# Optimization experiments

Hardware: AMD Instinct MI355X
Metric: run time of the kernel (lower is better)

Reference implementation:

```python
import jax, jax.numpy as jnp
import numpy as np

B, T1, T2 = 16, 1024, 1024
K1D, K2D, V1D, V2D, A = 512, 512, 256, 256, 128


def setup_inputs() -> dict:
    key = jax.random.key(0)
    ks = jax.random.split(key, 10)
    inp = {
        "k1": jax.random.normal(ks[0], (B, T1, K1D), dtype=jnp.float32),
        "k2": jax.random.normal(ks[1], (B, T2, K2D), dtype=jnp.float32),
        "v1": jax.random.normal(ks[2], (B, T1, V1D), dtype=jnp.float32),
        "v2": jax.random.normal(ks[3], (B, T2, V2D), dtype=jnp.float32),
        # Linear params (torch nn.Linear: y = x @ W.T + b)
        "W1": jax.random.normal(ks[4], (A, K1D), dtype=jnp.float32) / np.sqrt(K1D),
        "b1": jnp.zeros((A,), dtype=jnp.float32),
        "W2": jax.random.normal(ks[5], (A, K2D), dtype=jnp.float32) / np.sqrt(K2D),
        "b2": jnp.zeros((A,), dtype=jnp.float32),
        # valid lengths in [T/2, T-1] so no softmax row is entirely -inf
        "k1_lengths": jax.random.randint(ks[6], (B,), T1 // 2, T1, dtype=jnp.int32),
        "k2_lengths": jax.random.randint(ks[7], (B,), T2 // 2, T2, dtype=jnp.int32),
    }
    return inp


def reference(k1, k2, v1, v2, W1, b1, W2, b2, k1_lengths, k2_lengths):
    # projections
    q1 = jnp.einsum("bti,ai->bta", k1, W1) + b1  # [B,T1,A]
    q2 = jnp.einsum("bti,ai->bta", k2, W2) + b2  # [B,T2,A]
    # co-attention score [B,T1,T2]
    score = jnp.einsum("bia,bja->bij", q1, q2)
    # faithful mask: torch code adds 1 for rows>=l1 and 1 for cols>=l2,
    # then masks where sum == 1  -> XOR of the two pad conditions.
    row_pad = jnp.arange(T1)[None, :, None] >= k1_lengths[:, None, None]  # [B,T1,1]
    col_pad = jnp.arange(T2)[None, None, :] >= k2_lengths[:, None, None]  # [B,1,T2]
    mask = jnp.logical_xor(row_pad, col_pad)
    score = jnp.where(mask, -jnp.inf, score)
    # dual softmaxes
    w1 = jax.nn.softmax(jnp.swapaxes(score, 1, 2), axis=-1)  # [B,T2,T1]
    w2 = jax.nn.softmax(score, axis=-1)                      # [B,T1,T2]
    o1 = jnp.einsum("bji,bid->bjd", w1, v1)  # [B,T2,V1D]
    o2 = jnp.einsum("bij,bjd->bid", w2, v2)  # [B,T1,V2D]
    # note: the torch module additionally slices w1/w2/score per sample to
    # (l2,l1)/(l1,l2) ragged views; with fixed shapes we return the full
    # tensors (the valid region matches; slicing is a zero-copy view in torch).
    return (o1, o2, w1, w2, score)
```

## Files before the change

kernel.cpp:

```cpp
#include <hip/hip_runtime.h>
#include <math.h>

namespace {
constexpr int TT   = 1024;
constexpr int AD   = 128;
constexpr int KDIM = 512;
constexpr int VDIM = 256;
constexpr int NB   = 16;
constexpr size_t T2T = (size_t)TT * TT;
constexpr size_t BT  = (size_t)NB * TT;
}

#define MASK_VAL (-1.0e30f)

typedef __bf16 bf16x8 __attribute__((ext_vector_type(8)));
typedef float  f32x4  __attribute__((ext_vector_type(4)));

__device__ __forceinline__ unsigned short bf16_rne(float x) {
    unsigned int u = __builtin_bit_cast(unsigned int, x);
    u += 0x7fffu + ((u >> 16) & 1u);
    return (unsigned short)(u >> 16);
}
__device__ __forceinline__ float bf16f(unsigned short h) {
    return __builtin_bit_cast(float, ((unsigned int)h) << 16);
}
__device__ __forceinline__ void split2(float x, unsigned short& h, unsigned short& l) {
    h = bf16_rne(x);
    l = bf16_rne(x - bf16f(h));
}

__global__ __launch_bounds__(256) void prep_vt_kernel(
    const float* __restrict__ v1, const float* __restrict__ v2,
    unsigned short* __restrict__ vth, unsigned short* __restrict__ vtl)
{
    const int b     = blockIdx.x;
    const int k0    = blockIdx.y * 32;
    const int which = blockIdx.z;
    const float* vb = (which ? v1 : v2) + (size_t)b * TT * VDIM;
    const int tid = threadIdx.x;

    __shared__ float ls[32][257];
#pragma unroll
    for (int rep = 0; rep < 8; ++rep) {
        int idx = tid + rep * 256;
        int k  = idx >> 6;
        int n4 = (idx & 63) * 4;
        float4 x = *(const float4*)(vb + (size_t)(k0 + k) * VDIM + n4);
        ls[k][n4 + 0] = x.x;
        ls[k][n4 + 1] = x.y;
        ls[k][n4 + 2] = x.z;
        ls[k][n4 + 3] = x.w;
    }
    __syncthreads();

    const size_t pbase = ((size_t)(which * NB + b)) * VDIM * TT;
#pragma unroll
    for (int rep = 0; rep < 4; ++rep) {
        int idx = tid + rep * 256;
        int n  = idx >> 2;
        int sg = (idx & 3) * 8;
        unsigned short h[8], l[8];
#pragma unroll
        for (int j = 0; j < 8; ++j) {
            float x = ls[sg + j][n];
            split2(x, h[j], l[j]);
        }
        uint4 H, L;
        H.x = (unsigned)h[0] | ((unsigned)h[1] << 16);
        H.y = (unsigned)h[2] | ((unsigned)h[3] << 16);
        H.z = (unsigned)h[4] | ((unsigned)h[5] << 16);
        H.w = (unsigned)h[6] | ((unsigned)h[7] << 16);
        L.x = (unsigned)l[0] | ((unsigned)l[1] << 16);
        L.y = (unsigned)l[2] | ((unsigned)l[3] << 16);
        L.z = (unsigned)l[4] | ((unsigned)l[5] << 16);
        L.w = (unsigned)l[6] | ((unsigned)l[7] << 16);
        size_t off = pbase + (size_t)n * TT + k0 + sg;
        *(uint4*)(vth + off) = H;
        *(uint4*)(vtl + off) = L;
    }
}

__global__ __launch_bounds__(256) void qproj_mfma_kernel(
    const float* __restrict__ k1, const float* __restrict__ W1, const float* __restrict__ bias1,
    const float* __restrict__ k2, const float* __restrict__ W2, const float* __restrict__ bias2,
    unsigned short* __restrict__ q1h, unsigned short* __restrict__ q1l,
    unsigned short* __restrict__ q2h, unsigned short* __restrict__ q2l)
{
    const int proj = blockIdx.y;
    const float* __restrict__ K    = proj ? k2 : k1;
    const float* __restrict__ W    = proj ? W2 : W1;
    const float* __restrict__ bias = proj ? bias2 : bias1;
    unsigned short* __restrict__ qh = proj ? q2h : q1h;
    unsigned short* __restrict__ ql = proj ? q2l : q1l;

    const int m0 = blockIdx.x * 128;

    __shared__ alignas(16) unsigned short akh[128 * 40];
    __shared__ alignas(16) unsigned short akl[128 * 40];
    __shared__ alignas(16) unsigned short bwh[128 * 40];
    __shared__ alignas(16) unsigned short bwl[128 * 40];

    const int tid  = threadIdx.x;
    const int lane = tid & 63;
    const int wv   = tid >> 6;
    const int wm = wv >> 1, wn = wv & 1;
    const int la = lane & 15, kg = lane >> 4;

    f32x4 acc[4][4];
#pragma unroll
    for (int m = 0; m < 4; ++m)
#pragma unroll
        for (int n = 0; n < 4; ++n) acc[m][n] = (f32x4){0.f, 0.f, 0.f, 0.f};

    for (int k0 = 0; k0 < KDIM; k0 += 32) {
#pragma unroll
        for (int rep = 0; rep < 4; ++rep) {
            int idx = tid + rep * 256;
            int row = idx >> 3, c4 = (idx & 7) * 4;
            float4 x = *(const float4*)(K + (size_t)(m0 + row) * KDIM + k0 + c4);
            ushort4 H, L;
            split2(x.x, H.x, L.x);
            split2(x.y, H.y, L.y);
            split2(x.z, H.z, L.z);
            split2(x.w, H.w, L.w);
            *(ushort4*)&akh[row * 40 + c4] = H;
            *(ushort4*)&akl[row * 40 + c4] = L;
        }
#pragma unroll
        for (int rep = 0; rep < 4; ++rep) {
            int idx = tid + rep * 256;
            int row = idx >> 3, c4 = (idx & 7) * 4;
            float4 x = *(const float4*)(W + (size_t)row * KDIM + k0 + c4);
            ushort4 H, L;
            split2(x.x, H.x, L.x);
            split2(x.y, H.y, L.y);
            split2(x.z, H.z, L.z);
            split2(x.w, H.w, L.w);
            *(ushort4*)&bwh[row * 40 + c4] = H;
            *(ushort4*)&bwl[row * 40 + c4] = L;
        }
        __syncthreads();

        bf16x8 ah[4], al[4], bh[4], bl[4];
#pragma unroll
        for (int m = 0; m < 4; ++m) {
            int r = wm * 64 + m * 16 + la;
            ah[m] = *(const bf16x8*)&akh[r * 40 + kg * 8];
            al[m] = *(const bf16x8*)&akl[r * 40 + kg * 8];
        }
#pragma unroll
        for (int n = 0; n < 4; ++n) {
            int c = wn * 64 + n * 16 + la;
            bh[n] = *(const bf16x8*)&bwh[c * 40 + kg * 8];
            bl[n] = *(const bf16x8*)&bwl[c * 40 + kg * 8];
        }
#pragma unroll
        for (int m = 0; m < 4; ++m)
#pragma unroll
            for (int n = 0; n < 4; ++n) {
                acc[m][n] = __builtin_amdgcn_mfma_f32_16x16x32_bf16(ah[m], bh[n], acc[m][n], 0, 0, 0);
                acc[m][n] = __builtin_amdgcn_mfma_f32_16x16x32_bf16(ah[m], bl[n], acc[m][n], 0, 0, 0);
                acc[m][n] = __builtin_amdgcn_mfma_f32_16x16x32_bf16(al[m], bh[n], acc[m][n], 0, 0, 0);
            }
        __syncthreads();
    }

#pragma unroll
    for (int n = 0; n < 4; ++n) {
        int col = wn * 64 + n * 16 + la;
        float bv = bias[col];
#pragma unroll
        for (int m = 0; m < 4; ++m)
#pragma unroll
            for (int r = 0; r < 4; ++r) {
                int row = m0 + wm * 64 + m * 16 + kg * 4 + r;
                unsigned short h, l;
                split2(acc[m][n][r] + bv, h, l);
                qh[(size_t)row * AD + col] = h;
                ql[(size_t)row * AD + col] = l;
            }
    }
}

__global__ __launch_bounds__(256) void score_mfma_stats_kernel(
    const unsigned short* __restrict__ q1h, const unsigned short* __restrict__ q1l,
    const unsigned short* __restrict__ q2h, const unsigned short* __restrict__ q2l,
    const int* __restrict__ len1, const int* __restrict__ len2,
    float* __restrict__ score,
    float* __restrict__ prm, float* __restrict__ prs,
    float* __restrict__ pcm, float* __restrict__ pcs)
{
    const int b  = blockIdx.x;
    const int mt = blockIdx.y >> 3, nt = blockIdx.y & 7;
    const int m0 = mt * 128, n0 = nt * 128;
    const size_t qoff = (size_t)b * TT * AD;

    __shared__ alignas(16) unsigned short ath[128 * 40];
    __shared__ alignas(16) unsigned short atl[128 * 40];
    __shared__ alignas(16) unsigned short bth[128 * 40];
    __shared__ alignas(16) unsigned short btl[128 * 40];
    __shared__ float red_m[2][128];
    __shared__ float red_s[2][128];

    const int tid  = threadIdx.x;
    const int lane = tid & 63;
    const int wv   = tid >> 6;
    const int wm = wv >> 1, wn = wv & 1;
    const int la = lane & 15, kg = lane >> 4;

    f32x4 acc[4][4];
#pragma unroll
    for (int m = 0; m < 4; ++m)
#pragma unroll
        for (int n = 0; n < 4; ++n) acc[m][n] = (f32x4){0.f, 0.f, 0.f, 0.f};

    for (int k0 = 0; k0 < AD; k0 += 32) {
#pragma unroll
        for (int rep = 0; rep < 2; ++rep) {
            int idx = tid + rep * 256;
            int row = idx >> 2, sg = (idx & 3) * 8;
            *(uint4*)&ath[row * 40 + sg] = *(const uint4*)(q1h + qoff + (size_t)(m0 + row) * AD + k0 + sg);
            *(uint4*)&atl[row * 40 + sg] = *(const uint4*)(q1l + qoff + (size_t)(m0 + row) * AD + k0 + sg);
            *(uint4*)&bth[row * 40 + sg] = *(const uint4*)(q2h + qoff + (size_t)(n0 + row) * AD + k0 + sg);
            *(uint4*)&btl[row * 40 + sg] = *(const uint4*)(q2l + qoff + (size_t)(n0 + row) * AD + k0 + sg);
        }
        __syncthreads();

        bf16x8 ah[4], al[4], bh[4], bl[4];
#pragma unroll
        for (int m = 0; m < 4; ++m) {
            int r = wm * 64 + m * 16 + la;
            ah[m] = *(const bf16x8*)&ath[r * 40 + kg * 8];
            al[m] = *(const bf16x8*)&atl[r * 40 + kg * 8];
        }
#pragma unroll
        for (int n = 0; n < 4; ++n) {
            int c = wn * 64 + n * 16 + la;
            bh[n] = *(const bf16x8*)&bth[c * 40 + kg * 8];
            bl[n] = *(const bf16x8*)&btl[c * 40 + kg * 8];
        }
#pragma unroll
        for (int m = 0; m < 4; ++m)
#pragma unroll
            for (int n = 0; n < 4; ++n) {
                acc[m][n] = __builtin_amdgcn_mfma_f32_16x16x32_bf16(ah[m], bh[n], acc[m][n], 0, 0, 0);
                acc[m][n] = __builtin_amdgcn_mfma_f32_16x16x32_bf16(ah[m], bl[n], acc[m][n], 0, 0, 0);
                acc[m][n] = __builtin_amdgcn_mfma_f32_16x16x32_bf16(al[m], bh[n], acc[m][n], 0, 0, 0);
            }
        __syncthreads();
    }

    const int l1v = len1[b];
    const int l2v = len2[b];

#pragma unroll
    for (int m = 0; m < 4; ++m)
#pragma unroll
        for (int r = 0; r < 4; ++r) {
            int row = m0 + wm * 64 + m * 16 + kg * 4 + r;
            bool rp = row >= l1v;
#pragma unroll
            for (int n = 0; n < 4; ++n) {
                int col = n0 + wn * 64 + n * 16 + la;
                bool cp = col >= l2v;
                if (rp != cp) acc[m][n][r] = MASK_VAL;
            }
        }
    float* sb = score + (size_t)b * T2T;
#pragma unroll
    for (int m = 0; m < 4; ++m)
#pragma unroll
        for (int r = 0; r < 4; ++r) {
            int row = m0 + wm * 64 + m * 16 + kg * 4 + r;
#pragma unroll
            for (int n = 0; n < 4; ++n) {
                int col = n0 + wn * 64 + n * 16 + la;
                sb[(size_t)row * TT + col] = acc[m][n][r];
            }
        }

#pragma unroll
    for (int m = 0; m < 4; ++m)
#pragma unroll
        for (int r = 0; r < 4; ++r) {
            float mr = fmaxf(fmaxf(acc[m][0][r], acc[m][1][r]),
                             fmaxf(acc[m][2][r], acc[m][3][r]));
#pragma unroll
            for (int off = 1; off <= 8; off <<= 1) mr = fmaxf(mr, __shfl_xor(mr, off));
            float sr = __expf(acc[m][0][r] - mr) + __expf(acc[m][1][r] - mr) +
                       __expf(acc[m][2][r] - mr) + __expf(acc[m][3][r] - mr);
#pragma unroll
            for (int off = 1; off <= 8; off <<= 1) sr += __shfl_xor(sr, off);
            if (la == 0) {
                int rloc = wm * 64 + m * 16 + kg * 4 + r;
                red_m[wn][rloc] = mr;
                red_s[wn][rloc] = sr;
            }
        }
    __syncthreads();
    if (tid < 128) {
        float ma = red_m[0][tid], mb2 = red_m[1][tid];
        float mm = fmaxf(ma, mb2);
        float ss = red_s[0][tid] * __expf(ma - mm) + red_s[1][tid] * __expf(mb2 - mm);
        prm[(size_t)nt * BT + (size_t)b * TT + m0 + tid] = mm;
        prs[(size_t)nt * BT + (size_t)b * TT + m0 + tid] = ss;
    }
    __syncthreads();

#pragma unroll
    for (int n = 0; n < 4; ++n) {
        float mc = MASK_VAL;
#pragma unroll
        for (int m = 0; m < 4; ++m)
#pragma unroll
            for (int r = 0; r < 4; ++r) mc = fmaxf(mc, acc[m][n][r]);
#pragma unroll
        for (int off = 16; off <= 32; off <<= 1) mc = fmaxf(mc, __shfl_xor(mc, off));
        float sc = 0.f;
#pragma unroll
        for (int m = 0; m < 4; ++m)
#pragma unroll
            for (int r = 0; r < 4; ++r) sc += __expf(acc[m][n][r] - mc);
#pragma unroll
        for (int off = 16; off <= 32; off <<= 1) sc += __shfl_xor(sc, off);
        if (kg == 0) {
            int cloc = wn * 64 + n * 16 + la;
            red_m[wm][cloc] = mc;
            red_s[wm][cloc] = sc;
        }
    }
    __syncthreads();
    if (tid < 128) {
        float ma = red_m[0][tid], mb2 = red_m[1][tid];
        float mm = fmaxf(ma, mb2);
        float ss = red_s[0][tid] * __expf(ma - mm) + red_s[1][tid] * __expf(mb2 - mm);
        pcm[(size_t)mt * BT + (size_t)b * TT + n0 + tid] = mm;
        pcs[(size_t)mt * BT + (size_t)b * TT + n0 + tid] = ss;
    }
}

__global__ __launch_bounds__(256) void statcomb_kernel(
    const float* __restrict__ prm, const float* __restrict__ prs,
    const float* __restrict__ pcm, const float* __restrict__ pcs,
    float* __restrict__ rmax, float* __restrict__ rinv,
    float* __restrict__ cmax, float* __restrict__ cinv)
{
    const int id = blockIdx.x * 256 + threadIdx.x;
    const float* pm = blockIdx.y ? pcm : prm;
    const float* ps = blockIdx.y ? pcs : prs;
    float* om = blockIdx.y ? cmax : rmax;
    float* oi = blockIdx.y ? cinv : rinv;
    float nm = MASK_VAL;
#pragma unroll
    for (int c = 0; c < 8; ++c) nm = fmaxf(nm, pm[(size_t)c * BT + id]);
    float s = 0.f;
#pragma unroll
    for (int c = 0; c < 8; ++c)
        s += ps[(size_t)c * BT + id] * __expf(pm[(size_t)c * BT + id] - nm);
    om[id] = nm;
    oi[id] = 1.f / s;
}

__global__ __launch_bounds__(512) void ogemm_fused_kernel(
    const float* __restrict__ score,
    const float* __restrict__ rmax, const float* __restrict__ rinv,
    const float* __restrict__ cmax, const float* __restrict__ cinv,
    const unsigned short* __restrict__ vth, const unsigned short* __restrict__ vtl,
    float* __restrict__ w2, float* __restrict__ w1,
    float* __restrict__ o2, float* __restrict__ o1)
{
    const int b     = blockIdx.x;
    const int m0    = blockIdx.y * 128;
    const int which = blockIdx.z;
    const size_t vbase = ((size_t)(which * NB + b)) * VDIM * TT;

    const float* __restrict__ sb = score + (size_t)b * T2T;
    float* __restrict__ wout = (which ? w1 : w2) + (size_t)b * T2T;
    float* __restrict__ ob   = (which ? o1 : o2) + (size_t)b * TT * VDIM;

    __shared__ alignas(16) unsigned short awh[128 * 40];
    __shared__ alignas(16) unsigned short awl[128 * 40];
    __shared__ alignas(16) unsigned short bvh[256 * 40];
    __shared__ alignas(16) unsigned short bvl[256 * 40];
    __shared__ float st[128][33];
    __shared__ float sm_s[128], si_s[128];

    const int tid  = threadIdx.x;
    const int lane = tid & 63;
    const int wv   = tid >> 6;
    const int wm   = wv >> 2;
    const int wn   = wv & 3;
    const int la = lane & 15, kg = lane >> 4;

    if (tid < 128) {
        sm_s[tid] = (which ? cmax : rmax)[(size_t)b * TT + m0 + tid];
        si_s[tid] = (which ? cinv : rinv)[(size_t)b * TT + m0 + tid];
    }
    __syncthreads();

    f32x4 acc[4][4];
#pragma unroll
    for (int m = 0; m < 4; ++m)
#pragma unroll
        for (int n = 0; n < 4; ++n) acc[m][n] = (f32x4){0.f, 0.f, 0.f, 0.f};

    for (int k0 = 0; k0 < TT; k0 += 32) {
        if (which == 0) {
#pragma unroll
            for (int rep = 0; rep < 2; ++rep) {
                int idx = tid + rep * 512;
                int row = idx >> 3, c4 = (idx & 7) * 4;
                float4 x = *(const float4*)(sb + (size_t)(m0 + row) * TT + k0 + c4);
                float mm = sm_s[row], ii = si_s[row];
                f32x4 wv4;
                wv4[0] = __expf(x.x - mm) * ii;
                wv4[1] = __expf(x.y - mm) * ii;
                wv4[2] = __expf(x.z - mm) * ii;
                wv4[3] = __expf(x.w - mm) * ii;
                __builtin_nontemporal_store(wv4, (f32x4*)(wout + (size_t)(m0 + row) * TT + k0 + c4));
                ushort4 H, L;
                split2(wv4[0], H.x, L.x);
                split2(wv4[1], H.y, L.y);
                split2(wv4[2], H.z, L.z);
                split2(wv4[3], H.w, L.w);
                *(ushort4*)&awh[row * 40 + c4] = H;
                *(ushort4*)&awl[row * 40 + c4] = L;
            }
        } else {
#pragma unroll
            for (int rep = 0; rep < 2; ++rep) {
                int idx = tid + rep * 512;
                int ip = idx >> 5, c4 = (idx & 31) * 4;
                float4 x = *(const float4*)(sb + (size_t)(k0 + ip) * TT + m0 + c4);
                st[c4 + 0][ip] = __expf(x.x - sm_s[c4 + 0]) * si_s[c4 + 0];
                st[c4 + 1][ip] = __expf(x.y - sm_s[c4 + 1]) * si_s[c4 + 1];
                st[c4 + 2][ip] = __expf(x.z - sm_s[c4 + 2]) * si_s[c4 + 2];
                st[c4 + 3][ip] = __expf(x.w - sm_s[c4 + 3]) * si_s[c4 + 3];
            }
            __syncthreads();
#pragma unroll
            for (int rep = 0; rep < 2; ++rep) {
                int idx = tid + rep * 512;
                int j = idx >> 3, i4 = (idx & 7) * 4;
                f32x4 wv4;
                wv4[0] = st[j][i4 + 0];
                wv4[1] = st[j][i4 + 1];
                wv4[2] = st[j][i4 + 2];
                wv4[3] = st[j][i4 + 3];
                __builtin_nontemporal_store(wv4, (f32x4*)(wout + (size_t)(m0 + j) * TT + k0 + i4));
                ushort4 H, L;
                split2(wv4[0], H.x, L.x);
                split2(wv4[1], H.y, L.y);
                split2(wv4[2], H.z, L.z);
                split2(wv4[3], H.w, L.w);
                *(ushort4*)&awh[j * 40 + i4] = H;
                *(ushort4*)&awl[j * 40 + i4] = L;
            }
        }
#pragma unroll
        for (int rep = 0; rep < 2; ++rep) {
            int idx = tid + rep * 512;
            int n  = idx >> 2;
            int sg = (idx & 3) * 8;
            size_t off = vbase + (size_t)n * TT + k0 + sg;
            *(uint4*)&bvh[n * 40 + sg] = *(const uint4*)(vth + off);
            *(uint4*)&bvl[n * 40 + sg] = *(const uint4*)(vtl + off);
        }
        __syncthreads();

        bf16x8 ah[4], al[4], bh[4], bl[4];
#pragma unroll
        for (int m = 0; m < 4; ++m) {
            int r = wm * 64 + m * 16 + la;
            ah[m] = *(const bf16x8*)&awh[r * 40 + kg * 8];
            al[m] = *(const bf16x8*)&awl[r * 40 + kg * 8];
        }
#pragma unroll
        for (int n = 0; n < 4; ++n) {
            int c = wn * 64 + n * 16 + la;
            bh[n] = *(const bf16x8*)&bvh[c * 40 + kg * 8];
            bl[n] = *(const bf16x8*)&bvl[c * 40 + kg * 8];
        }
#pragma unroll
        for (int m = 0; m < 4; ++m)
#pragma unroll
            for (int n = 0; n < 4; ++n) {
                acc[m][n] = __builtin_amdgcn_mfma_f32_16x16x32_bf16(ah[m], bh[n], acc[m][n], 0, 0, 0);
                acc[m][n] = __builtin_amdgcn_mfma_f32_16x16x32_bf16(ah[m], bl[n], acc[m][n], 0, 0, 0);
                acc[m][n] = __builtin_amdgcn_mfma_f32_16x16x32_bf16(al[m], bh[n], acc[m][n], 0, 0, 0);
            }
        __syncthreads();
    }

#pragma unroll
    for (int m = 0; m < 4; ++m)
#pragma unroll
        for (int r = 0; r < 4; ++r) {
            int row = m0 + wm * 64 + m * 16 + kg * 4 + r;
#pragma unroll
            for (int n = 0; n < 4; ++n) {
                int col = wn * 64 + n * 16 + la;
                __builtin_nontemporal_store(acc[m][n][r], ob + (size_t)row * VDIM + col);
            }
        }
}

extern "C" void kernel_launch(void* const* d_in, const int* in_sizes, int n_in,
                              void* d_out, int out_size, void* d_ws, size_t ws_size,
                              hipStream_t stream) {
    const float* k1 = (const float*)d_in[0];
    const float* k2 = (const float*)d_in[1];
    const float* v1 = (const float*)d_in[2];
    const float* v2 = (const float*)d_in[3];
    const float* W1 = (const float*)d_in[4];
    const float* b1 = (const float*)d_in[5];
    const float* W2 = (const float*)d_in[6];
    const float* b2 = (const float*)d_in[7];
    const int* len1 = (const int*)d_in[8];
    const int* len2 = (const int*)d_in[9];

    float* out = (float*)d_out;
    float* o1    = out;
    float* o2    = out + (size_t)NB * TT * VDIM;
    float* w1    = out + (size_t)2 * NB * TT * VDIM;
    float* w2    = w1 + (size_t)NB * T2T;
    float* score = w2 + (size_t)NB * T2T;

    float* ws   = (float*)d_ws;
    float* rmax = ws;
    float* rinv = rmax + BT;
    float* cmax = rinv + BT;
    float* cinv = cmax + BT;
    float* prm  = cinv + BT;
    float* prs  = prm + 8 * BT;
    float* pcm  = prs + 8 * BT;
    float* pcs  = pcm + 8 * BT;
    unsigned short* q1h = (unsigned short*)(pcs + 8 * BT);
    unsigned short* q1l = q1h + BT * AD;
    unsigned short* q2h = q1l + BT * AD;
    unsigned short* q2l = q2h + BT * AD;
    unsigned short* vth = q2l + BT * AD;
    unsigned short* vtl = vth + (size_t)32 * VDIM * TT;

    prep_vt_kernel<<<dim3(NB, TT / 32, 2), 256, 0, stream>>>(v1, v2, vth, vtl);
    qproj_mfma_kernel<<<dim3(NB * TT / 128, 2), 256, 0, stream>>>(k1, W1, b1, k2, W2, b2,
                                                                  q1h, q1l, q2h, q2l);
    score_mfma_stats_kernel<<<dim3(NB, 64), 256, 0, stream>>>(q1h, q1l, q2h, q2l,
                                                              len1, len2, score,
                                                              prm, prs, pcm, pcs);
    statcomb_kernel<<<dim3(BT / 256, 2), 256, 0, stream>>>(prm, prs, pcm, pcs,
                                                           rmax, rinv, cmax, cinv);
    ogemm_fused_kernel<<<dim3(NB, TT / 128, 2), 512, 0, stream>>>(score, rmax, rinv, cmax, cinv,
                                                                  vth, vtl, w2, w1, o2, o1);
}
```

Baseline: 179.5 us.

## Load MFMA operands directly from global and software-prefetch score and V tiles

The score kernel now loads the q1/q2 hi/lo bf16 fragments straight from global memory into registers instead of staging them through LDS. This removes the per-step shared-memory round trips and barriers. In the output kernel the V^T hi/lo fragments are likewise read directly into registers, and both the score tile and the V fragments for the next k-step are issued one iteration ahead so their latency overlaps the current exp and MFMA work. This adds register pressure, and the global reads are duplicated across waves (each wave loads its own fragments, so there is less reuse than with shared staging).

```diff
diff --git a/kernel.cpp b/kernel.cpp
--- a/kernel.cpp
+++ b/kernel.cpp
@@ -27,6 +27,9 @@
 __device__ __forceinline__ void split2(float x, unsigned short& h, unsigned short& l) {
     h = bf16_rne(x);
     l = bf16_rne(x - bf16f(h));
+}
+__device__ __forceinline__ bf16x8 as_bf16x8(uint4 u) {
+    return __builtin_bit_cast(bf16x8, u);
 }
 
 __global__ __launch_bounds__(256) void prep_vt_kernel(
@@ -195,10 +198,6 @@
     const int m0 = mt * 128, n0 = nt * 128;
     const size_t qoff = (size_t)b * TT * AD;
 
-    __shared__ alignas(16) unsigned short ath[128 * 40];
-    __shared__ alignas(16) unsigned short atl[128 * 40];
-    __shared__ alignas(16) unsigned short bth[128 * 40];
-    __shared__ alignas(16) unsigned short btl[128 * 40];
     __shared__ float red_m[2][128];
     __shared__ float red_s[2][128];
 
@@ -214,30 +213,20 @@
 #pragma unroll
         for (int n = 0; n < 4; ++n) acc[m][n] = (f32x4){0.f, 0.f, 0.f, 0.f};
 
+#pragma unroll
     for (int k0 = 0; k0 < AD; k0 += 32) {
-#pragma unroll
-        for (int rep = 0; rep < 2; ++rep) {
-            int idx = tid + rep * 256;
-            int row = idx >> 2, sg = (idx & 3) * 8;
-            *(uint4*)&ath[row * 40 + sg] = *(const uint4*)(q1h + qoff + (size_t)(m0 + row) * AD + k0 + sg);
-            *(uint4*)&atl[row * 40 + sg] = *(const uint4*)(q1l + qoff + (size_t)(m0 + row) * AD + k0 + sg);
-            *(uint4*)&bth[row * 40 + sg] = *(const uint4*)(q2h + qoff + (size_t)(n0 + row) * AD + k0 + sg);
-            *(uint4*)&btl[row * 40 + sg] = *(const uint4*)(q2l + qoff + (size_t)(n0 + row) * AD + k0 + sg);
-        }
-        __syncthreads();
-
         bf16x8 ah[4], al[4], bh[4], bl[4];
 #pragma unroll
         for (int m = 0; m < 4; ++m) {
-            int r = wm * 64 + m * 16 + la;
-            ah[m] = *(const bf16x8*)&ath[r * 40 + kg * 8];
-            al[m] = *(const bf16x8*)&atl[r * 40 + kg * 8];
+            size_t off = qoff + (size_t)(m0 + wm * 64 + m * 16 + la) * AD + k0 + kg * 8;
+            ah[m] = as_bf16x8(*(const uint4*)(q1h + off));
+            al[m] = as_bf16x8(*(const uint4*)(q1l + off));
         }
 #pragma unroll
         for (int n = 0; n < 4; ++n) {
-            int c = wn * 64 + n * 16 + la;
-            bh[n] = *(const bf16x8*)&bth[c * 40 + kg * 8];
-            bl[n] = *(const bf16x8*)&btl[c * 40 + kg * 8];
+            size_t off = qoff + (size_t)(n0 + wn * 64 + n * 16 + la) * AD + k0 + kg * 8;
+            bh[n] = as_bf16x8(*(const uint4*)(q2h + off));
+            bl[n] = as_bf16x8(*(const uint4*)(q2l + off));
         }
 #pragma unroll
         for (int m = 0; m < 4; ++m)
@@ -247,7 +236,6 @@
                 acc[m][n] = __builtin_amdgcn_mfma_f32_16x16x32_bf16(ah[m], bl[n], acc[m][n], 0, 0, 0);
                 acc[m][n] = __builtin_amdgcn_mfma_f32_16x16x32_bf16(al[m], bh[n], acc[m][n], 0, 0, 0);
             }
-        __syncthreads();
     }
 
     const int l1v = len1[b];
@@ -380,8 +368,6 @@
 
     __shared__ alignas(16) unsigned short awh[128 * 40];
     __shared__ alignas(16) unsigned short awl[128 * 40];
-    __shared__ alignas(16) unsigned short bvh[256 * 40];
-    __shared__ alignas(16) unsigned short bvl[256 * 40];
     __shared__ float st[128][33];
     __shared__ float sm_s[128], si_s[128];
 
@@ -392,6 +378,11 @@
     const int wn   = wv & 3;
     const int la = lane & 15, kg = lane >> 4;
 
+    const int r_row0 = tid >> 3,          r_c4_0 = (tid & 7) * 4;
+    const int r_row1 = (tid + 512) >> 3,  r_c4_1 = ((tid + 512) & 7) * 4;
+    const int c_ip0 = tid >> 5,           c_c4_0 = (tid & 31) * 4;
+    const int c_ip1 = (tid + 512) >> 5,   c_c4_1 = ((tid + 512) & 31) * 4;
+
     if (tid < 128) {
         sm_s[tid] = (which ? cmax : rmax)[(size_t)b * TT + m0 + tid];
         si_s[tid] = (which ? cinv : rinv)[(size_t)b * TT + m0 + tid];
@@ -404,13 +395,37 @@
 #pragma unroll
         for (int n = 0; n < 4; ++n) acc[m][n] = (f32x4){0.f, 0.f, 0.f, 0.f};
 
+    float4 aA0, aA1;
+    uint4  bhr[4], blr[4];
+
+    auto issueA = [&](int k0) {
+        if (which == 0) {
+            aA0 = *(const float4*)(sb + (size_t)(m0 + r_row0) * TT + k0 + r_c4_0);
+            aA1 = *(const float4*)(sb + (size_t)(m0 + r_row1) * TT + k0 + r_c4_1);
+        } else {
+            aA0 = *(const float4*)(sb + (size_t)(k0 + c_ip0) * TT + m0 + c_c4_0);
+            aA1 = *(const float4*)(sb + (size_t)(k0 + c_ip1) * TT + m0 + c_c4_1);
+        }
+    };
+    auto issueB = [&](int k0) {
+#pragma unroll
+        for (int n = 0; n < 4; ++n) {
+            size_t off = vbase + (size_t)(wn * 64 + n * 16 + la) * TT + k0 + kg * 8;
+            bhr[n] = *(const uint4*)(vth + off);
+            blr[n] = *(const uint4*)(vtl + off);
+        }
+    };
+
+    issueA(0);
+    issueB(0);
+
     for (int k0 = 0; k0 < TT; k0 += 32) {
         if (which == 0) {
 #pragma unroll
             for (int rep = 0; rep < 2; ++rep) {
-                int idx = tid + rep * 512;
-                int row = idx >> 3, c4 = (idx & 7) * 4;
-                float4 x = *(const float4*)(sb + (size_t)(m0 + row) * TT + k0 + c4);
+                float4 x = rep ? aA1 : aA0;
+                int row = rep ? r_row1 : r_row0;
+                int c4  = rep ? r_c4_1 : r_c4_0;
                 float mm = sm_s[row], ii = si_s[row];
                 f32x4 wv4;
                 wv4[0] = __expf(x.x - mm) * ii;
@@ -426,17 +441,22 @@
                 *(ushort4*)&awh[row * 40 + c4] = H;
                 *(ushort4*)&awl[row * 40 + c4] = L;
             }
+            if (k0 + 32 < TT) issueA(k0 + 32);
+            __syncthreads();
         } else {
-#pragma unroll
-            for (int rep = 0; rep < 2; ++rep) {
-                int idx = tid + rep * 512;
-                int ip = idx >> 5, c4 = (idx & 31) * 4;
-                float4 x = *(const float4*)(sb + (size_t)(k0 + ip) * TT + m0 + c4);
-                st[c4 + 0][ip] = __expf(x.x - sm_s[c4 + 0]) * si_s[c4 + 0];
-                st[c4 + 1][ip] = __expf(x.y - sm_s[c4 + 1]) * si_s[c4 + 1];
-                st[c4 + 2][ip] = __expf(x.z - sm_s[c4 + 2]) * si_s[c4 + 2];
-                st[c4 + 3][ip] = __expf(x.w - sm_s[c4 + 3]) * si_s[c4 + 3];
-            }
+            {
+                float4 x = aA0;
+                st[c_c4_0 + 0][c_ip0] = __expf(x.x - sm_s[c_c4_0 + 0]) * si_s[c_c4_0 + 0];
+                st[c_c4_0 + 1][c_ip0] = __expf(x.y - sm_s[c_c4_0 + 1]) * si_s[c_c4_0 + 1];
+                st[c_c4_0 + 2][c_ip0] = __expf(x.z - sm_s[c_c4_0 + 2]) * si_s[c_c4_0 + 2];
+                st[c_c4_0 + 3][c_ip0] = __expf(x.w - sm_s[c_c4_0 + 3]) * si_s[c_c4_0 + 3];
+                x = aA1;
+                st[c_c4_1 + 0][c_ip1] = __expf(x.x - sm_s[c_c4_1 + 0]) * si_s[c_c4_1 + 0];
+                st[c_c4_1 + 1][c_ip1] = __expf(x.y - sm_s[c_c4_1 + 1]) * si_s[c_c4_1 + 1];
+                st[c_c4_1 + 2][c_ip1] = __expf(x.z - sm_s[c_c4_1 + 2]) * si_s[c_c4_1 + 2];
+                st[c_c4_1 + 3][c_ip1] = __expf(x.w - sm_s[c_c4_1 + 3]) * si_s[c_c4_1 + 3];
+            }
+            if (k0 + 32 < TT) issueA(k0 + 32);
             __syncthreads();
 #pragma unroll
             for (int rep = 0; rep < 2; ++rep) {
@@ -456,19 +476,10 @@
                 *(ushort4*)&awh[j * 40 + i4] = H;
                 *(ushort4*)&awl[j * 40 + i4] = L;
             }
-        }
-#pragma unroll
-        for (int rep = 0; rep < 2; ++rep) {
-            int idx = tid + rep * 512;
-            int n  = idx >> 2;
-            int sg = (idx & 3) * 8;
-            size_t off = vbase + (size_t)n * TT + k0 + sg;
-            *(uint4*)&bvh[n * 40 + sg] = *(const uint4*)(vth + off);
-            *(uint4*)&bvl[n * 40 + sg] = *(const uint4*)(vtl + off);
-        }
-        __syncthreads();
-
-        bf16x8 ah[4], al[4], bh[4], bl[4];
+            __syncthreads();
+        }
+
+        bf16x8 ah[4], al[4];
 #pragma unroll
         for (int m = 0; m < 4; ++m) {
             int r = wm * 64 + m * 16 + la;
@@ -476,19 +487,16 @@
             al[m] = *(const bf16x8*)&awl[r * 40 + kg * 8];
         }
 #pragma unroll
-        for (int n = 0; n < 4; ++n) {
-            int c = wn * 64 + n * 16 + la;
-            bh[n] = *(const bf16x8*)&bvh[c * 40 + kg * 8];
-            bl[n] = *(const bf16x8*)&bvl[c * 40 + kg * 8];
-        }
-#pragma unroll
         for (int m = 0; m < 4; ++m)
 #pragma unroll
             for (int n = 0; n < 4; ++n) {
-                acc[m][n] = __builtin_amdgcn_mfma_f32_16x16x32_bf16(ah[m], bh[n], acc[m][n], 0, 0, 0);
-                acc[m][n] = __builtin_amdgcn_mfma_f32_16x16x32_bf16(ah[m], bl[n], acc[m][n], 0, 0, 0);
-                acc[m][n] = __builtin_amdgcn_mfma_f32_16x16x32_bf16(al[m], bh[n], acc[m][n], 0, 0, 0);
-            }
+                bf16x8 bh = as_bf16x8(bhr[n]);
+                bf16x8 bl = as_bf16x8(blr[n]);
+                acc[m][n] = __builtin_amdgcn_mfma_f32_16x16x32_bf16(ah[m], bh, acc[m][n], 0, 0, 0);
+                acc[m][n] = __builtin_amdgcn_mfma_f32_16x16x32_bf16(ah[m], bl, acc[m][n], 0, 0, 0);
+                acc[m][n] = __builtin_amdgcn_mfma_f32_16x16x32_bf16(al[m], bh, acc[m][n], 0, 0, 0);
+            }
+        if (k0 + 32 < TT) issueB(k0 + 32);
         __syncthreads();
     }
 
```

New measurement: 221.8 us. +23.5%, slower.
